# Kernel tuning notes

Hardware: AMD Instinct MI355X
Metric: run time of the kernel (lower is better)

The kernel has to match this reference:

```python
import jax, jax.numpy as jnp
import numpy as np

B, T, C, H = 4, 4096, 1024, 64

def setup_inputs() -> dict:
    key = jax.random.key(0)
    k1, k2, k3, k4 = jax.random.split(key, 4)
    x = jax.random.normal(k1, (B, T, C), dtype=jnp.float32)
    # nn.Linear(C, H, bias=False): y = x @ W^T with W [H, C]; store as [C, H] for x @ W
    Wq = jax.random.normal(k2, (C, H), dtype=jnp.float32) * (C ** -0.5)
    Wk = jax.random.normal(k3, (C, H), dtype=jnp.float32) * (C ** -0.5)
    Wv = jax.random.normal(k4, (C, H), dtype=jnp.float32) * (C ** -0.5)
    return {"x": x, "Wq": Wq, "Wk": Wk, "Wv": Wv}

def reference(x, Wq, Wk, Wv):
    # Manual causal single-head attention (dropout p=0 -> identity).
    q = x @ Wq  # [B, T, H]
    k = x @ Wk  # [B, T, H]
    v = x @ Wv  # [B, T, H]
    scale = q.shape[-1] ** -0.5
    w = jnp.einsum('bth,bsh->bts', q, k) * scale  # [B, T, T] scores
    causal = jnp.tril(jnp.ones((x.shape[1], x.shape[1]), dtype=bool))
    w = jnp.where(causal, w, -jnp.inf)
    w = jax.nn.softmax(w, axis=-1)
    out = jnp.einsum('bts,bsh->bth', w, v)  # [B, T, H]
    return out
```

## Files before the change

### kernel.cpp

```cpp
#include <hip/hip_runtime.h>
#include <math.h>

#define Bn 4
#define Tn 4096
#define Cn 1024
#define Hn 64

typedef __attribute__((ext_vector_type(8))) short short8;
typedef __attribute__((ext_vector_type(4))) float floatx4;
typedef unsigned short ushort_t;

#define QSCALE 0.1803368801111204f

__device__ __forceinline__ ushort_t f2bf(float f) {
  union { float f; unsigned u; } v; v.f = f;
  unsigned r = v.u + 0x7FFFu + ((v.u >> 16) & 1u);
  return (ushort_t)(r >> 16);
}
__device__ __forceinline__ ushort_t f2bf_hu(float f) {
  union { float f; unsigned u; } v; v.f = f;
  return (ushort_t)((v.u + 0x8000u) >> 16);
}
__device__ __forceinline__ float bf2f(ushort_t h) {
  union { unsigned u; float f; } v; v.u = ((unsigned)h) << 16; return v.f;
}


__global__ __launch_bounds__(256) void wf_kernel(
    const float* __restrict__ Wq, const float* __restrict__ Wk,
    const float* __restrict__ Wv, ushort_t* __restrict__ Wf)
{
  __shared__ float ws[32][65];
  const int tid = threadIdx.x;
  const int m = blockIdx.x >> 5;
  const int g = blockIdx.x & 31;
  const float* W = (m == 0) ? Wq : (m == 1) ? Wk : Wv;
  const float4* src = (const float4*)(W + (size_t)g * 32 * Hn);
#pragma unroll
  for (int it = 0; it < 2; ++it) {
    int i4 = it * 256 + tid;
    float4 v = src[i4];
    int c = i4 >> 4, h = (i4 & 15) * 4;
    ws[c][h] = v.x; ws[c][h + 1] = v.y; ws[c][h + 2] = v.z; ws[c][h + 3] = v.w;
  }
  __syncthreads();
  const int nt = tid >> 6, lane = tid & 63;
  const int col = lane & 15, quad = lane >> 4;
  ushort_t t[8];
#pragma unroll
  for (int e = 0; e < 8; ++e) t[e] = f2bf(ws[quad * 8 + e][nt * 16 + col]);
  *(short8*)(Wf + ((size_t)((m * 32 + g) * 4 + nt) * 64 + lane) * 8) = *(short8*)t;
}

__global__ __launch_bounds__(256, 2) void qkv_proj_kernel(
    const float* __restrict__ x, const ushort_t* __restrict__ Wf,
    ushort_t* __restrict__ Qf, ushort_t* __restrict__ Kf,
    ushort_t* __restrict__ Vf)
{
  __shared__ __align__(16) char smem[67584];
  ushort_t* xs  = (ushort_t*)smem;
  ushort_t* red = (ushort_t*)smem;
  ushort_t* img = (ushort_t*)(smem + 49152);

  const int tid  = threadIdx.x;
  const int wv   = tid >> 6;
  const int lane = tid & 63;
  const int col  = lane & 15;
  const int quad = lane >> 4;
  const int blk  = blockIdx.x;
  const int row0 = blk * 32;

#define BF_LOAD(DST, GG)                                                        \
  do {                                                                          \
    _Pragma("unroll")                                                           \
    for (int k = 0; k < 12; ++k) {                                              \
      const int m_ = k >> 2, nt_ = k & 3;                                       \
      DST[k] = *(const short8*)(Wf + ((size_t)((m_ * 32 + (GG)) * 4 + nt_) * 64 + lane) * 8); \
    }                                                                           \
  } while (0)

  short8 bfA[12], bfB[12];
  BF_LOAD(bfA, wv * 8);

#pragma unroll
  for (int half = 0; half < 2; ++half) {
    float4 v[16];
#pragma unroll
    for (int jj = 0; jj < 16; ++jj)
      v[jj] = *(const float4*)(x + (size_t)(row0 + half * 16 + jj) * Cn + wv * 256 + lane * 4);
#pragma unroll
    for (int jj = 0; jj < 16; ++jj) {
      ushort4 u;
      u.x = f2bf(v[jj].x); u.y = f2bf(v[jj].y); u.z = f2bf(v[jj].z); u.w = f2bf(v[jj].w);
      *(ushort4*)(xs + (wv * 32 + half * 16 + jj) * 264 + lane * 4) = u;
    }
  }

  floatx4 acc[2][3][4];
#pragma unroll
  for (int sub = 0; sub < 2; ++sub)
#pragma unroll
    for (int m = 0; m < 3; ++m)
#pragma unroll
      for (int nt = 0; nt < 4; ++nt) {
        acc[sub][m][nt][0] = 0.f; acc[sub][m][nt][1] = 0.f;
        acc[sub][m][nt][2] = 0.f; acc[sub][m][nt][3] = 0.f;
      }

#define QKV_MFMA(BF, CH)                                                        \
  do {                                                                          \
    short8 af0 = *(const short8*)(xs + (wv * 32 + col) * 264 + (CH) * 32 + quad * 8);        \
    short8 af1 = *(const short8*)(xs + (wv * 32 + 16 + col) * 264 + (CH) * 32 + quad * 8);   \
    _Pragma("unroll")                                                           \
    for (int k = 0; k < 12; ++k) {                                              \
      const int m_ = k >> 2, nt_ = k & 3;                                       \
      acc[0][m_][nt_] = __builtin_amdgcn_mfma_f32_16x16x32_bf16(af0, BF[k], acc[0][m_][nt_], 0, 0, 0); \
      acc[1][m_][nt_] = __builtin_amdgcn_mfma_f32_16x16x32_bf16(af1, BF[k], acc[1][m_][nt_], 0, 0, 0); \
    }                                                                           \
  } while (0)

#pragma unroll
  for (int ch2 = 0; ch2 < 4; ++ch2) {
    const int ch = ch2 * 2;
    BF_LOAD(bfB, wv * 8 + ch + 1);
    QKV_MFMA(bfA, ch);
    if (ch2 < 3) BF_LOAD(bfA, wv * 8 + ch + 2);
    QKV_MFMA(bfB, ch + 1);
  }
  __syncthreads();

#pragma unroll
  for (int sub = 0; sub < 2; ++sub)
#pragma unroll
    for (int m = 0; m < 3; ++m)
#pragma unroll
      for (int nt = 0; nt < 4; ++nt) {
        const int p = (sub * 3 + m) * 4 + nt;
        ushort4 u;
        u.x = f2bf(acc[sub][m][nt][0]); u.y = f2bf(acc[sub][m][nt][1]);
        u.z = f2bf(acc[sub][m][nt][2]); u.w = f2bf(acc[sub][m][nt][3]);
        *(ushort4*)&red[((p * 4 + wv) * 64 + lane) * 4] = u;
      }
  __syncthreads();

#pragma unroll
  for (int pp = 0; pp < 6; ++pp) {
    const int p = wv * 6 + pp;
    ushort4 w0 = *(const ushort4*)&red[((p * 4 + 0) * 64 + lane) * 4];
    ushort4 w1 = *(const ushort4*)&red[((p * 4 + 1) * 64 + lane) * 4];
    ushort4 w2 = *(const ushort4*)&red[((p * 4 + 2) * 64 + lane) * 4];
    ushort4 w3 = *(const ushort4*)&red[((p * 4 + 3) * 64 + lane) * 4];
    float v[4];
    v[0] = (bf2f(w0.x) + bf2f(w1.x)) + (bf2f(w2.x) + bf2f(w3.x));
    v[1] = (bf2f(w0.y) + bf2f(w1.y)) + (bf2f(w2.y) + bf2f(w3.y));
    v[2] = (bf2f(w0.z) + bf2f(w1.z)) + (bf2f(w2.z) + bf2f(w3.z));
    v[3] = (bf2f(w0.w) + bf2f(w1.w)) + (bf2f(w2.w) + bf2f(w3.w));
    const int sub = (p >= 12) ? 1 : 0;
    const int mrem = p - sub * 12;
    const int m = mrem >> 2, nt = mrem & 3;
#pragma unroll
    for (int r = 0; r < 4; ++r) {
      const int tlq = quad * 4 + r;
      if (m == 2) {
        img[4096 + nt * 512 + (quad * 16 + col) * 8 + sub * 4 + r] = f2bf(v[r]);
      } else {
        const int h = nt * 16 + col;
        const int idx = (h >> 5) * 512 + ((h >> 3) & 3) * 128 + tlq * 8 + (h & 7);
        img[m * 2048 + sub * 1024 + idx] = f2bf(m == 0 ? v[r] * QSCALE : v[r]);
      }
    }
  }
  __syncthreads();

  {
    const int b = blk >> 7, g = blk & 127;
#pragma unroll
    for (int sub = 0; sub < 2; ++sub) {
      const size_t qg = (size_t)(b * 256 + 2 * g + sub) * 1024 + tid * 4;
      *(uint2*)(Qf + qg) = *(const uint2*)&img[sub * 1024 + tid * 4];
      *(uint2*)(Kf + qg) = *(const uint2*)&img[2048 + sub * 1024 + tid * 4];
    }
    const int ht = tid >> 6;
    const size_t vg = ((size_t)(b * 64 + (g >> 1)) * 8 + ht * 2 + (g & 1)) * 512 + (tid & 63) * 8;
    *(short8*)(Vf + vg) = *(const short8*)&img[4096 + ht * 512 + (tid & 63) * 8];
  }
}

__global__ __launch_bounds__(256, 2) void attn_kernel(
    const ushort_t* __restrict__ Qf, const ushort_t* __restrict__ Kf,
    const ushort_t* __restrict__ Vf, float* __restrict__ out)
{
  __shared__ __align__(16) float Om[4][2][16][68];
  __shared__ __align__(16) float Ml[4][2][16];

  const int tid  = threadIdx.x;
  const int wv   = tid >> 6;
  const int lane = tid & 63;
  const int col  = lane & 15;
  const int quad = lane >> 4;
  const int b   = blockIdx.x & 3;
  const int idx = blockIdx.x >> 2;
  const int g   = (idx < 64) ? (127 - 2 * idx) : (2 * (idx - 64));

  short8 qf[2][2];
#pragma unroll
  for (int sub = 0; sub < 2; ++sub)
#pragma unroll
    for (int half = 0; half < 2; ++half)
      qf[sub][half] = *(const short8*)(Qf + (size_t)(b * 256 + 2 * g + sub) * 1024 + half * 512 + lane * 8);

  const ushort_t* Kbase = Kf + (size_t)b * 256 * 1024;
  const ushort_t* Vbase = Vf + (size_t)b * 64 * 8 * 512;

  short8 ones;
#pragma unroll
  for (int e = 0; e < 8; ++e) ones[e] = (short)0x3F80;

  floatx4 o[2][4], ol[2];
#pragma unroll
  for (int sub = 0; sub < 2; ++sub) {
#pragma unroll
    for (int ht = 0; ht < 4; ++ht) { o[sub][ht][0]=0.f; o[sub][ht][1]=0.f; o[sub][ht][2]=0.f; o[sub][ht][3]=0.f; }
    ol[sub][0]=0.f; ol[sub][1]=0.f; ol[sub][2]=0.f; ol[sub][3]=0.f;
  }

  const int ntile = ((g * 32 + 31) >> 6) + 1;
  const int dtile = ntile - 1;

  short8 kfA[8], vfA[8], kfB[8], vfB[8];

#define LOADKV(KF, VF, II)                                                      \
  do {                                                                          \
    _Pragma("unroll")                                                           \
    for (int kt = 0; kt < 4; ++kt) {                                            \
      const ushort_t* kp = Kbase + (size_t)(II) * 4096 + kt * 1024 + lane * 8;  \
      KF[kt * 2]     = *(const short8*)(kp);                                    \
      KF[kt * 2 + 1] = *(const short8*)(kp + 512);                              \
    }                                                                           \
    _Pragma("unroll")                                                           \
    for (int ht = 0; ht < 4; ++ht) {                                            \
      _Pragma("unroll")                                                         \
      for (int kh = 0; kh < 2; ++kh)                                            \
        VF[ht * 2 + kh] = *(const short8*)(Vbase + ((size_t)(II) * 8 + ht * 2 + kh) * 512 + lane * 8); \
    }                                                                           \
  } while (0)

#define TILE_BODY(KF, VF, II)                                                   \
  do {                                                                          \
    floatx4 s[2][4];                                                            \
    __builtin_amdgcn_s_setprio(1);                                              \
    _Pragma("unroll")                                                           \
    for (int sub = 0; sub < 2; ++sub)                                           \
      _Pragma("unroll")                                                         \
      for (int kt = 0; kt < 4; ++kt) {                                          \
        floatx4 c; c[0]=0.f; c[1]=0.f; c[2]=0.f; c[3]=0.f;                      \
        c = __builtin_amdgcn_mfma_f32_16x16x32_bf16(KF[kt * 2],     qf[sub][0], c, 0, 0, 0); \
        c = __builtin_amdgcn_mfma_f32_16x16x32_bf16(KF[kt * 2 + 1], qf[sub][1], c, 0, 0, 0); \
        s[sub][kt] = c;                                                         \
      }                                                                         \
    __builtin_amdgcn_s_setprio(0);                                              \
    if ((II) == dtile) {                                                        \
      _Pragma("unroll")                                                         \
      for (int sub = 0; sub < 2; ++sub)                                         \
        _Pragma("unroll")                                                       \
        for (int kt = 0; kt < 4; ++kt)                                          \
          _Pragma("unroll")                                                     \
          for (int r = 0; r < 4; ++r)                                           \
            if (64 * (II) + kt * 16 + quad * 4 + r > g * 32 + sub * 16 + col)   \
              s[sub][kt][r] = -INFINITY;                                        \
    }                                                                           \
    _Pragma("unroll")                                                           \
    for (int sub = 0; sub < 2; ++sub)                                           \
      _Pragma("unroll")                                                         \
      for (int kt = 0; kt < 4; ++kt)                                            \
        _Pragma("unroll")                                                       \
        for (int r = 0; r < 4; ++r)                                             \
          s[sub][kt][r] = __builtin_amdgcn_exp2f(s[sub][kt][r]);                \
    short8 pf[2][2];                                                            \
    _Pragma("unroll")                                                           \
    for (int sub = 0; sub < 2; ++sub)                                           \
      _Pragma("unroll")                                                         \
      for (int kh = 0; kh < 2; ++kh) {                                          \
        ushort_t tmp[8];                                                        \
        _Pragma("unroll")                                                       \
        for (int half = 0; half < 2; ++half)                                    \
          _Pragma("unroll")                                                     \
          for (int r = 0; r < 4; ++r)                                           \
            tmp[half * 4 + r] = f2bf_hu(s[sub][2 * kh + half][r]);              \
        pf[sub][kh] = *(short8*)tmp;                                            \
      }                                                                         \
    __builtin_amdgcn_s_setprio(1);                                              \
    _Pragma("unroll")                                                           \
    for (int sub = 0; sub < 2; ++sub) {                                         \
      _Pragma("unroll")                                                         \
      for (int ht = 0; ht < 4; ++ht) {                                          \
        o[sub][ht] = __builtin_amdgcn_mfma_f32_16x16x32_bf16(pf[sub][0], VF[ht * 2],     o[sub][ht], 0, 0, 0); \
        o[sub][ht] = __builtin_amdgcn_mfma_f32_16x16x32_bf16(pf[sub][1], VF[ht * 2 + 1], o[sub][ht], 0, 0, 0); \
      }                                                                         \
      ol[sub] = __builtin_amdgcn_mfma_f32_16x16x32_bf16(pf[sub][0], ones, ol[sub], 0, 0, 0); \
      ol[sub] = __builtin_amdgcn_mfma_f32_16x16x32_bf16(pf[sub][1], ones, ol[sub], 0, 0, 0); \
    }                                                                           \
    __builtin_amdgcn_s_setprio(0);                                              \
  } while (0)

  {
    int i = wv;
    if (i < ntile) LOADKV(kfA, vfA, i);
    while (i < ntile) {
      int j = i + 4;
      if (j < ntile) LOADKV(kfB, vfB, j);
      TILE_BODY(kfA, vfA, i);
      i = j;
      if (i >= ntile) break;
      j = i + 4;
      if (j < ntile) LOADKV(kfA, vfA, j);
      TILE_BODY(kfB, vfB, i);
      i = j;
    }
  }

#pragma unroll
  for (int sub = 0; sub < 2; ++sub) {
#pragma unroll
    for (int ht = 0; ht < 4; ++ht)
#pragma unroll
      for (int r = 0; r < 4; ++r)
        Om[wv][sub][quad * 4 + r][ht * 16 + col] = o[sub][ht][r];
    if (col == 0) {
#pragma unroll
      for (int r = 0; r < 4; ++r) Ml[wv][sub][quad * 4 + r] = ol[sub][r];
    }
  }
  __syncthreads();

  const int rr = tid >> 4, h4 = (tid & 15) * 4;
#pragma unroll
  for (int sub = 0; sub < 2; ++sub) {
    float L = (Ml[0][sub][rr] + Ml[1][sub][rr]) + (Ml[2][sub][rr] + Ml[3][sub][rr]);
    float4 a; a.x = 0.f; a.y = 0.f; a.z = 0.f; a.w = 0.f;
#pragma unroll
    for (int w = 0; w < 4; ++w) {
      float4 ov = *(const float4*)&Om[w][sub][rr][h4];
      a.x += ov.x; a.y += ov.y; a.z += ov.z; a.w += ov.w;
    }
    float inv = 1.f / L;
    a.x *= inv; a.y *= inv; a.z *= inv; a.w *= inv;
    *(float4*)(out + (size_t)(b * Tn + g * 32 + sub * 16 + rr) * Hn + h4) = a;
  }
}

extern "C" void kernel_launch(void* const* d_in, const int* in_sizes, int n_in,
                              void* d_out, int out_size, void* d_ws, size_t ws_size,
                              hipStream_t stream) {
  const float* x  = (const float*)d_in[0];
  const float* Wq = (const float*)d_in[1];
  const float* Wk = (const float*)d_in[2];
  const float* Wv = (const float*)d_in[3];
  float* out = (float*)d_out;

  ushort_t* Qf = (ushort_t*)d_ws;
  ushort_t* Kf = Qf + (size_t)Bn * Tn * Hn;
  ushort_t* Vf = Kf + (size_t)Bn * Tn * Hn;
  ushort_t* Wf = Vf + (size_t)Bn * Tn * Hn;

  wf_kernel<<<dim3(96), dim3(256), 0, stream>>>(Wq, Wk, Wv, Wf);
  qkv_proj_kernel<<<dim3(512), dim3(256), 0, stream>>>(x, Wf, Qf, Kf, Vf);
  attn_kernel<<<dim3(Bn * 128), dim3(256), 0, stream>>>(Qf, Kf, Vf, out);
}
```

Before: 129.6 us.

## Replace cross-iteration KV prefetch with paired-tile loads and per-sub softmax staging

```diff
diff --git a/kernel.cpp b/kernel.cpp
--- a/kernel.cpp
+++ b/kernel.cpp
@@ -227,8 +227,6 @@
   const int ntile = ((g * 32 + 31) >> 6) + 1;
   const int dtile = ntile - 1;
 
-  short8 kfA[8], vfA[8], kfB[8], vfB[8];
-
 #define LOADKV(KF, VF, II)                                                      \
   do {                                                                          \
     _Pragma("unroll")                                                           \
@@ -247,38 +245,32 @@
 
 #define TILE_BODY(KF, VF, II)                                                   \
   do {                                                                          \
-    floatx4 s[2][4];                                                            \
-    __builtin_amdgcn_s_setprio(1);                                              \
-    _Pragma("unroll")                                                           \
-    for (int sub = 0; sub < 2; ++sub)                                           \
+    _Pragma("unroll")                                                           \
+    for (int sub = 0; sub < 2; ++sub) {                                         \
+      floatx4 s[4];                                                             \
+      __builtin_amdgcn_s_setprio(1);                                            \
       _Pragma("unroll")                                                         \
       for (int kt = 0; kt < 4; ++kt) {                                          \
         floatx4 c; c[0]=0.f; c[1]=0.f; c[2]=0.f; c[3]=0.f;                      \
         c = __builtin_amdgcn_mfma_f32_16x16x32_bf16(KF[kt * 2],     qf[sub][0], c, 0, 0, 0); \
         c = __builtin_amdgcn_mfma_f32_16x16x32_bf16(KF[kt * 2 + 1], qf[sub][1], c, 0, 0, 0); \
-        s[sub][kt] = c;                                                         \
+        s[kt] = c;                                                              \
       }                                                                         \
-    __builtin_amdgcn_s_setprio(0);                                              \
-    if ((II) == dtile) {                                                        \
-      _Pragma("unroll")                                                         \
-      for (int sub = 0; sub < 2; ++sub)                                         \
+      __builtin_amdgcn_s_setprio(0);                                            \
+      if ((II) == dtile) {                                                      \
         _Pragma("unroll")                                                       \
         for (int kt = 0; kt < 4; ++kt)                                          \
           _Pragma("unroll")                                                     \
           for (int r = 0; r < 4; ++r)                                           \
             if (64 * (II) + kt * 16 + quad * 4 + r > g * 32 + sub * 16 + col)   \
-              s[sub][kt][r] = -INFINITY;                                        \
-    }                                                                           \
-    _Pragma("unroll")                                                           \
-    for (int sub = 0; sub < 2; ++sub)                                           \
+              s[kt][r] = -INFINITY;                                             \
+      }                                                                         \
       _Pragma("unroll")                                                         \
       for (int kt = 0; kt < 4; ++kt)                                            \
         _Pragma("unroll")                                                       \
         for (int r = 0; r < 4; ++r)                                             \
-          s[sub][kt][r] = __builtin_amdgcn_exp2f(s[sub][kt][r]);                \
-    short8 pf[2][2];                                                            \
-    _Pragma("unroll")                                                           \
-    for (int sub = 0; sub < 2; ++sub)                                           \
+          s[kt][r] = __builtin_amdgcn_exp2f(s[kt][r]);                          \
+      short8 pf[2];                                                             \
       _Pragma("unroll")                                                         \
       for (int kh = 0; kh < 2; ++kh) {                                          \
         ushort_t tmp[8];                                                        \
@@ -286,37 +278,29 @@
         for (int half = 0; half < 2; ++half)                                    \
           _Pragma("unroll")                                                     \
           for (int r = 0; r < 4; ++r)                                           \
-            tmp[half * 4 + r] = f2bf_hu(s[sub][2 * kh + half][r]);              \
-        pf[sub][kh] = *(short8*)tmp;                                            \
+            tmp[half * 4 + r] = f2bf_hu(s[2 * kh + half][r]);                   \
+        pf[kh] = *(short8*)tmp;                                                 \
       }                                                                         \
-    __builtin_amdgcn_s_setprio(1);                                              \
-    _Pragma("unroll")                                                           \
-    for (int sub = 0; sub < 2; ++sub) {                                         \
+      __builtin_amdgcn_s_setprio(1);                                            \
       _Pragma("unroll")                                                         \
       for (int ht = 0; ht < 4; ++ht) {                                          \
-        o[sub][ht] = __builtin_amdgcn_mfma_f32_16x16x32_bf16(pf[sub][0], VF[ht * 2],     o[sub][ht], 0, 0, 0); \
-        o[sub][ht] = __builtin_amdgcn_mfma_f32_16x16x32_bf16(pf[sub][1], VF[ht * 2 + 1], o[sub][ht], 0, 0, 0); \
+        o[sub][ht] = __builtin_amdgcn_mfma_f32_16x16x32_bf16(pf[0], VF[ht * 2],     o[sub][ht], 0, 0, 0); \
+        o[sub][ht] = __builtin_amdgcn_mfma_f32_16x16x32_bf16(pf[1], VF[ht * 2 + 1], o[sub][ht], 0, 0, 0); \
       }                                                                         \
-      ol[sub] = __builtin_amdgcn_mfma_f32_16x16x32_bf16(pf[sub][0], ones, ol[sub], 0, 0, 0); \
-      ol[sub] = __builtin_amdgcn_mfma_f32_16x16x32_bf16(pf[sub][1], ones, ol[sub], 0, 0, 0); \
-    }                                                                           \
-    __builtin_amdgcn_s_setprio(0);                                              \
+      ol[sub] = __builtin_amdgcn_mfma_f32_16x16x32_bf16(pf[0], ones, ol[sub], 0, 0, 0); \
+      ol[sub] = __builtin_amdgcn_mfma_f32_16x16x32_bf16(pf[1], ones, ol[sub], 0, 0, 0); \
+      __builtin_amdgcn_s_setprio(0);                                            \
+    }                                                                           \
   } while (0)
 
-  {
-    int i = wv;
-    if (i < ntile) LOADKV(kfA, vfA, i);
-    while (i < ntile) {
-      int j = i + 4;
-      if (j < ntile) LOADKV(kfB, vfB, j);
-      TILE_BODY(kfA, vfA, i);
-      i = j;
-      if (i >= ntile) break;
-      j = i + 4;
-      if (j < ntile) LOADKV(kfA, vfA, j);
-      TILE_BODY(kfB, vfB, i);
-      i = j;
-    }
+  for (int i0 = wv * 2; i0 < ntile; i0 += 8) {
+    short8 kfa[8], vfa[8], kfb[8], vfb[8];
+    const int i1 = i0 + 1;
+    const bool h2 = (i1 < ntile);
+    LOADKV(kfa, vfa, i0);
+    if (h2) LOADKV(kfb, vfb, i1);
+    TILE_BODY(kfa, vfa, i0);
+    if (h2) TILE_BODY(kfb, vfb, i1);
   }
 
 #pragma unroll
```

After: 129.4 us. About the same (-0.1%).
